# Performance work log

Measured on AMD Instinct MI355X. Metric: run time of the kernel, lower is better.

Reference implementation:

```python
import jax, jax.numpy as jnp
import numpy as np

N = 512   # speakers
M = 64    # samples per speaker
D = 768   # embedding dim
EPS = 1e-8  # torch F.cosine_similarity eps


def setup_inputs() -> dict:
    key = jax.random.key(0)
    k1, = jax.random.split(key, 1)
    speaker_vectors = jax.random.normal(k1, (N * M, D), dtype=jnp.float32)
    w = jnp.asarray(10.0, dtype=jnp.float32)
    b = jnp.asarray(-5.0, dtype=jnp.float32)
    return {"speaker_vectors": speaker_vectors, "w": w, "b": b}


def _cosine(a, b):
    # torch F.cosine_similarity: a.b / (max(|a|,eps) * max(|b|,eps)), over last dim
    na = jnp.maximum(jnp.linalg.norm(a, axis=-1), EPS)
    nb = jnp.maximum(jnp.linalg.norm(b, axis=-1), EPS)
    return jnp.sum(a * b, axis=-1) / (na * nb)


def reference(speaker_vectors, w, b):
    x = speaker_vectors.reshape(N, M, D)            # [N, M, D]
    sums = x.sum(axis=1)                            # [N, D]
    centroids = sums / M                            # [N, D]
    excl = (sums[:, None, :] - x) / (M - 1)         # exclusive centroids [N, M, D]

    # cosine sim of every centroid against every sample: [N_centroid, N_spk, M]
    xn = jnp.maximum(jnp.linalg.norm(x, axis=-1), EPS)          # [N, M]
    cn = jnp.maximum(jnp.linalg.norm(centroids, axis=-1), EPS)  # [N]
    dots = jnp.einsum('nd,imd->nim', centroids, x)              # [N, N, M]
    S = w * (dots / (cn[:, None, None] * xn[None])) + b         # [N, N, M]

    # same-speaker entries use the leave-one-out centroid
    S_same = w * _cosine(excl, x) + b               # [N, M]
    idx = jnp.arange(N)
    S = S.at[idx, idx].set(S_same)                  # overwrite diagonal block

    # L_j = -S_same_j + log sum_n exp(S[n, j])
    L = -S_same + jax.scipy.special.logsumexp(S, axis=0)  # [N, M]
    return L.sum()
```

## Files before the change

kernel.cpp:

```cpp
#include <hip/hip_runtime.h>
#include <hip/hip_bf16.h>
#include <math.h>

#define EPS 1e-8f

typedef __attribute__((ext_vector_type(2))) unsigned long ulongx2;
typedef __attribute__((ext_vector_type(4))) float floatx4;
typedef unsigned char uchar_t;

#define GPTR(p) ((const __attribute__((address_space(1))) void*)(p))
#define LPTR(p) ((__attribute__((address_space(3))) void*)(p))

__device__ __forceinline__ unsigned int pk4(float a, float b, float c, float d) {
  int v = __builtin_amdgcn_cvt_pk_fp8_f32(a, b, 0, false);
  v = __builtin_amdgcn_cvt_pk_fp8_f32(c, d, v, true);
  return (unsigned int)v;
}

__global__ __launch_bounds__(512, 4) void kA(const float* __restrict__ x,
    uchar_t* __restrict__ xbf8fm, float* __restrict__ sums_f32,
    float* __restrict__ ss, float* __restrict__ rcn,
    float* __restrict__ xx, float* __restrict__ rxn,
    const float* __restrict__ wp) {
  const int n = blockIdx.x;
  const int t = threadIdx.x;
  const int wv = t >> 6, l = t & 63;
  __shared__ uchar_t xs[64][776];
  __shared__ float rqp[64][65];
  __shared__ float red8[8];

  float4 cs[3] = {{0,0,0,0},{0,0,0,0},{0,0,0,0}};
  for (int c = 0; c < 2; ++c) {
    float4 v[4][3];
#pragma unroll
    for (int rr = 0; rr < 4; ++rr) {
      const int r = wv * 8 + c * 4 + rr;
      const float* rp = x + ((size_t)n * 64 + r) * 768 + l * 4;
#pragma unroll
      for (int q = 0; q < 3; ++q) v[rr][q] = *(const float4*)(rp + q * 256);
    }
#pragma unroll
    for (int rr = 0; rr < 4; ++rr) {
      const int r = wv * 8 + c * 4 + rr;
      float rq = 0.f;
#pragma unroll
      for (int q = 0; q < 3; ++q) {
        const float4 u = v[rr][q];
        *(unsigned int*)&xs[r][l * 4 + q * 256] = pk4(u.x, u.y, u.z, u.w);
        rq += u.x*u.x + u.y*u.y + u.z*u.z + u.w*u.w;
        cs[q].x += u.x; cs[q].y += u.y; cs[q].z += u.z; cs[q].w += u.w;
      }
      rqp[r][l] = rq;
    }
  }
  __syncthreads();

  {
    const int gg = wv >> 1;
    const int half = wv & 1;
    const int g = n * 4 + gg;
#pragma unroll
    for (int ksi = 0; ksi < 6; ++ksi) {
      const int ks = half * 6 + ksi;
      const uchar_t* sp = &xs[gg * 16 + (l & 15)][ks * 64 + (l >> 4) * 8];
      uint2 lo = *(const uint2*)sp;
      uint2 hi = *(const uint2*)(sp + 32);
      uint4 outv = {lo.x, lo.y, hi.x, hi.y};
      *(uint4*)(xbf8fm + (size_t)((g * 12 + ks) * 64 + l) * 16) = outv;
    }
  }

  {
    const int r = t >> 3;
    const int o = (t & 7) * 8;
    float s = 0.f;
#pragma unroll
    for (int i = 0; i < 8; ++i) s += rqp[r][o + i];
    s += __shfl_xor(s, 1, 64);
    s += __shfl_xor(s, 2, 64);
    s += __shfl_xor(s, 4, 64);
    if ((t & 7) == 0) {
      const int j = n * 64 + r;
      xx[j] = s;
      rxn[j] = 1.0f / fmaxf(sqrtf(s), EPS);
    }
  }
  __syncthreads();

  float (*csum)[768] = (float (*)[768])&xs[0][0];
#pragma unroll
  for (int q = 0; q < 3; ++q)
    *(floatx4*)&csum[wv][l * 4 + q * 256] = (floatx4){cs[q].x, cs[q].y, cs[q].z, cs[q].w};
  __syncthreads();

  float lss = 0.f;
  {
    const int c0 = t;
    float s0 = 0.f;
#pragma unroll
    for (int w = 0; w < 8; ++w) s0 += csum[w][c0];
    sums_f32[(size_t)n * 768 + c0] = s0;
    lss += s0 * s0;
    if (t < 256) {
      const int c1 = 512 + t;
      float s1 = 0.f;
#pragma unroll
      for (int w = 0; w < 8; ++w) s1 += csum[w][c1];
      sums_f32[(size_t)n * 768 + c1] = s1;
      lss += s1 * s1;
    }
  }
  for (int o = 32; o; o >>= 1) lss += __shfl_xor(lss, o, 64);
  if (l == 0) red8[wv] = lss;
  __syncthreads();
  if (t == 0) {
    float vv = 0.f;
#pragma unroll
    for (int w = 0; w < 8; ++w) vv += red8[w];
    ss[n] = vv;
    rcn[n] = (*wp) / fmaxf(sqrtf(vv), 64.f * EPS);
  }
}

__global__ __launch_bounds__(256) void kA2(const float* __restrict__ sums_f32,
    uchar_t* __restrict__ sums8fm) {
  const int g = blockIdx.x;
  const int wv = threadIdx.x >> 6, l = threadIdx.x & 63;
#pragma unroll
  for (int ksi = 0; ksi < 3; ++ksi) {
    const int ks = wv * 3 + ksi;
    const float* sp = sums_f32 + (size_t)(g * 16 + (l & 15)) * 768
                      + ks * 64 + (l >> 4) * 8;
    float4 a0 = *(const float4*)sp;
    float4 a1 = *(const float4*)(sp + 4);
    float4 b0 = *(const float4*)(sp + 32);
    float4 b1 = *(const float4*)(sp + 36);
    uint4 outv = { pk4(a0.x, a0.y, a0.z, a0.w), pk4(a1.x, a1.y, a1.z, a1.w),
                   pk4(b0.x, b0.y, b0.z, b0.w), pk4(b1.x, b1.y, b1.z, b1.w) };
    *(uint4*)(sums8fm + (size_t)((g * 12 + ks) * 64 + l) * 16) = outv;
  }
}

__global__ __launch_bounds__(512, 2) void kC(const uchar_t* __restrict__ xbf8fm,
    const uchar_t* __restrict__ sums8fm, const float* __restrict__ rcn,
    const float* __restrict__ rxn, float* __restrict__ colsum_part,
    float* __restrict__ sdiag_dot, const float* __restrict__ bp) {
  __shared__ uchar_t lds[4][32768];
  const int b = blockIdx.x;
  const int xcd = b & 7;
  const int inner = b >> 3;
  const int nt = inner & 1;
  const int jt = xcd + ((inner >> 1) << 3);
  const int n0 = nt * 256, j0 = jt * 256;
  const int t = threadIdx.x, wv = t >> 6, l = t & 63;
  const int wm = wv >> 2, wj = wv & 3;
  const int gA0 = n0 / 16, gB0 = j0 / 16;

#define STAGE(KS_, BUF_) {                                                     \
    const int fb0_ = wv * 2, fb1_ = wv * 2 + 1;                                \
    __builtin_amdgcn_global_load_lds(                                          \
        GPTR(sums8fm + (size_t)(((gA0 + fb0_) * 12 + (KS_)) * 64 + l) * 16),   \
        LPTR(&lds[BUF_][fb0_ * 1024]), 16, 0, 0);                              \
    __builtin_amdgcn_global_load_lds(                                          \
        GPTR(sums8fm + (size_t)(((gA0 + fb1_) * 12 + (KS_)) * 64 + l) * 16),   \
        LPTR(&lds[BUF_][fb1_ * 1024]), 16, 0, 0);                              \
    __builtin_amdgcn_global_load_lds(                                          \
        GPTR(xbf8fm + (size_t)(((gB0 + fb0_) * 12 + (KS_)) * 64 + l) * 16),    \
        LPTR(&lds[BUF_][16384 + fb0_ * 1024]), 16, 0, 0);                      \
    __builtin_amdgcn_global_load_lds(                                          \
        GPTR(xbf8fm + (size_t)(((gB0 + fb1_) * 12 + (KS_)) * 64 + l) * 16),    \
        LPTR(&lds[BUF_][16384 + fb1_ * 1024]), 16, 0, 0);                      \
  }

  floatx4 acc[8][4];
#pragma unroll
  for (int mi = 0; mi < 8; ++mi)
#pragma unroll
    for (int ni = 0; ni < 4; ++ni) acc[mi][ni] = (floatx4){0.f, 0.f, 0.f, 0.f};

  STAGE(0, 0)
  STAGE(1, 1)
  STAGE(2, 2)

  for (int kb = 0; kb < 12; ++kb) {
    if (kb < 10)       { asm volatile("s_waitcnt vmcnt(8)" ::: "memory"); }
    else if (kb == 10) { asm volatile("s_waitcnt vmcnt(4)" ::: "memory"); }
    else               { asm volatile("s_waitcnt vmcnt(0)" ::: "memory"); }
    __builtin_amdgcn_s_barrier();
    __builtin_amdgcn_sched_barrier(0);
    const int cb = kb & 3, sb = (kb + 3) & 3;

    ulongx2 af[8], bf[4];
#pragma unroll
    for (int ni = 0; ni < 4; ++ni)
      bf[ni] = *(const ulongx2*)&lds[cb][16384 + (wj * 4 + ni) * 1024 + l * 16];
#pragma unroll
    for (int mi = 0; mi < 8; ++mi)
      af[mi] = *(const ulongx2*)&lds[cb][(wm * 8 + mi) * 1024 + l * 16];
    if (kb + 3 < 12) STAGE(kb + 3, sb)
    __builtin_amdgcn_s_setprio(1);
#pragma unroll
    for (int mi = 0; mi < 8; ++mi)
#pragma unroll
      for (int ni = 0; ni < 4; ++ni) {
        acc[mi][ni] = __builtin_amdgcn_mfma_f32_16x16x32_fp8_fp8(
            (long)af[mi].x, (long)bf[ni].x, acc[mi][ni], 0, 0, 0);
        acc[mi][ni] = __builtin_amdgcn_mfma_f32_16x16x32_fp8_fp8(
            (long)af[mi].y, (long)bf[ni].y, acc[mi][ni], 0, 0, 0);
      }
    __builtin_amdgcn_s_setprio(0);
  }

  const float bb = *bp;
  float rxv[4], p[4] = {0.f, 0.f, 0.f, 0.f};
#pragma unroll
  for (int ni = 0; ni < 4; ++ni)
    rxv[ni] = rxn[j0 + wj * 64 + ni * 16 + (l & 15)];
  const bool diagblk = (nt == (jt >> 6));

#pragma unroll
  for (int mi = 0; mi < 8; ++mi) {
    float4 rr = *(const float4*)&rcn[n0 + wm * 128 + mi * 16 + ((l >> 4) << 2)];
    const float rc[4] = {rr.x, rr.y, rr.z, rr.w};
#pragma unroll
    for (int ni = 0; ni < 4; ++ni) {
      floatx4 a = acc[mi][ni];
#pragma unroll
      for (int q = 0; q < 4; ++q)
        p[ni] += __expf(a[q] * rc[q] * rxv[ni] + bb);
      if (diagblk) {
        const int jg = j0 + wj * 64 + ni * 16 + (l & 15);
#pragma unroll
        for (int q = 0; q < 4; ++q) {
          const int mg = n0 + wm * 128 + mi * 16 + ((l >> 4) << 2) + q;
          if (mg == (jg >> 6)) sdiag_dot[jg] = a[q];
        }
      }
    }
  }
#pragma unroll
  for (int ni = 0; ni < 4; ++ni) {
    p[ni] += __shfl_xor(p[ni], 16, 64);
    p[ni] += __shfl_xor(p[ni], 32, 64);
  }
  if (l < 16) {
    const int slot = nt * 2 + wm;
#pragma unroll
    for (int ni = 0; ni < 4; ++ni)
      colsum_part[(size_t)slot * 32768 + j0 + wj * 64 + ni * 16 + l] = p[ni];
  }
}

__global__ __launch_bounds__(256) void kD(const float* __restrict__ colsum_part,
    const float* __restrict__ sdiag_dot, const float* __restrict__ xx,
    const float* __restrict__ ss, const float* __restrict__ rcn,
    const float* __restrict__ wp, const float* __restrict__ bp,
    float* __restrict__ partial) {
  const int j = blockIdx.x * 256 + threadIdx.x;
  const int i = j >> 6;
  const float ww = *wp, bb = *bp;
  const float sx = sdiag_dot[j];
  const float xxv = xx[j];
  const float xn = fmaxf(sqrtf(xxv), EPS);
  const float rx = 1.0f / xn;
  const float sd = sx * rcn[i] * rx + bb;
  const float exn = sqrtf(fmaxf(ss[i] - 2.f * sx + xxv, 0.f)) * (1.f / 63.f);
  const float edot = (sx - xxv) * (1.f / 63.f);
  const float sm = ww * edot / (fmaxf(exn, EPS) * xn) + bb;
  const float cssum = colsum_part[j] + colsum_part[32768 + j]
                    + colsum_part[65536 + j] + colsum_part[98304 + j];
  const float tot = cssum - __expf(sd) + __expf(sm);
  float L = -sm + logf(fmaxf(tot, 1e-30f));
  for (int o = 32; o; o >>= 1) L += __shfl_xor(L, o, 64);
  __shared__ float red[4];
  if ((threadIdx.x & 63) == 0) red[threadIdx.x >> 6] = L;
  __syncthreads();
  if (threadIdx.x == 0)
    partial[blockIdx.x] = red[0] + red[1] + red[2] + red[3];
}

__global__ __launch_bounds__(128) void kE(const float* __restrict__ partial,
    float* __restrict__ out) {
  const int t = threadIdx.x;
  float v = partial[t];
  for (int o = 32; o; o >>= 1) v += __shfl_xor(v, o, 64);
  __shared__ float r2[2];
  if ((t & 63) == 0) r2[t >> 6] = v;
  __syncthreads();
  if (t == 0) out[0] = r2[0] + r2[1];
}

extern "C" void kernel_launch(void* const* d_in, const int* in_sizes, int n_in,
                              void* d_out, int out_size, void* d_ws, size_t ws_size,
                              hipStream_t stream) {
  const float* x  = (const float*)d_in[0];
  const float* wp = (const float*)d_in[1];
  const float* bp = (const float*)d_in[2];
  float* out = (float*)d_out;

  float* fws = (float*)d_ws;
  float* ss          = fws;
  float* rcn         = fws + 512;
  float* xx          = fws + 1024;
  float* rxn         = fws + 33792;
  float* colsum_part = fws + 66560;
  float* sdiag_dot   = fws + 197632;
  float* partial     = fws + 230400;
  float* sums_f32    = fws + 230528;
  uchar_t* sums8fm   = (uchar_t*)(fws + 623744);
  uchar_t* xbf8fm    = (uchar_t*)(fws + 722048);

  kA<<<512, 512, 0, stream>>>(x, xbf8fm, sums_f32, ss, rcn, xx, rxn, wp);
  kA2<<<32, 256, 0, stream>>>(sums_f32, sums8fm);
  kC<<<256, 512, 0, stream>>>(xbf8fm, sums8fm, rcn, rxn, colsum_part, sdiag_dot, bp);
  kD<<<128, 256, 0, stream>>>(colsum_part, sdiag_dot, xx, ss, rcn, wp, bp, partial);
  kE<<<1, 128, 0, stream>>>(partial, out);
}
```

Measured before the change: 52.12 us.

## Stream prep-kernel rows through double-buffered async global-to-LDS loads

The prep kernel now streams its 64 rows in eight chunks of 8 using global_load_lds DMA into a two-slot float LDS buffer. Each chunk is converted to fp8 and reduced (squared norms, column sums) while the next chunk loads, so memory latency overlaps with compute. The fp8 fragment-major stores move inside the loop, every 16 rows, using a smaller 16-row staging buffer. This adds LDS footprint, manual waitcnt and barrier handling, and extra barriers per pair of chunks, and it relies on per-wave buffer ownership being safe without full syncs.

```diff
diff --git a/kernel.cpp b/kernel.cpp
--- a/kernel.cpp
+++ b/kernel.cpp
@@ -25,48 +25,69 @@
   const int n = blockIdx.x;
   const int t = threadIdx.x;
   const int wv = t >> 6, l = t & 63;
-  __shared__ uchar_t xs[64][776];
+  __shared__ float fbuf[2][8][768];
+  __shared__ uchar_t xs[16][776];
   __shared__ float rqp[64][65];
   __shared__ float red8[8];
 
+  const float* xbase = x + (size_t)n * 64 * 768;
+
+#define DMA(C_) {                                                              \
+    const float* src_ = xbase + (size_t)((C_) * 8 + wv) * 768 + l * 4;         \
+    __builtin_amdgcn_global_load_lds(GPTR(src_),                               \
+        LPTR(&fbuf[(C_) & 1][wv][0]), 16, 0, 0);                               \
+    __builtin_amdgcn_global_load_lds(GPTR(src_ + 256),                         \
+        LPTR(&fbuf[(C_) & 1][wv][256]), 16, 0, 0);                             \
+    __builtin_amdgcn_global_load_lds(GPTR(src_ + 512),                         \
+        LPTR(&fbuf[(C_) & 1][wv][512]), 16, 0, 0);                             \
+  }
+
   float4 cs[3] = {{0,0,0,0},{0,0,0,0},{0,0,0,0}};
-  for (int c = 0; c < 2; ++c) {
-    float4 v[4][3];
-#pragma unroll
-    for (int rr = 0; rr < 4; ++rr) {
-      const int r = wv * 8 + c * 4 + rr;
-      const float* rp = x + ((size_t)n * 64 + r) * 768 + l * 4;
-#pragma unroll
-      for (int q = 0; q < 3; ++q) v[rr][q] = *(const float4*)(rp + q * 256);
-    }
-#pragma unroll
-    for (int rr = 0; rr < 4; ++rr) {
-      const int r = wv * 8 + c * 4 + rr;
-      float rq = 0.f;
-#pragma unroll
-      for (int q = 0; q < 3; ++q) {
-        const float4 u = v[rr][q];
-        *(unsigned int*)&xs[r][l * 4 + q * 256] = pk4(u.x, u.y, u.z, u.w);
-        rq += u.x*u.x + u.y*u.y + u.z*u.z + u.w*u.w;
-        cs[q].x += u.x; cs[q].y += u.y; cs[q].z += u.z; cs[q].w += u.w;
+  DMA(0)
+
+  for (int c = 0; c < 8; ++c) {
+    if (c < 7) { DMA(c + 1) asm volatile("s_waitcnt vmcnt(3)" ::: "memory"); }
+    else       { asm volatile("s_waitcnt vmcnt(0)" ::: "memory"); }
+    __builtin_amdgcn_sched_barrier(0);
+
+    {
+      const float* fr = &fbuf[c & 1][wv][0];
+      float4 v0 = *(const float4*)(fr + l * 4);
+      float4 v1 = *(const float4*)(fr + l * 4 + 256);
+      float4 v2 = *(const float4*)(fr + l * 4 + 512);
+      const int xr = (c & 1) * 8 + wv;
+      *(unsigned int*)&xs[xr][l * 4]       = pk4(v0.x, v0.y, v0.z, v0.w);
+      *(unsigned int*)&xs[xr][l * 4 + 256] = pk4(v1.x, v1.y, v1.z, v1.w);
+      *(unsigned int*)&xs[xr][l * 4 + 512] = pk4(v2.x, v2.y, v2.z, v2.w);
+      float rq = v0.x*v0.x + v0.y*v0.y + v0.z*v0.z + v0.w*v0.w
+               + v1.x*v1.x + v1.y*v1.y + v1.z*v1.z + v1.w*v1.w
+               + v2.x*v2.x + v2.y*v2.y + v2.z*v2.z + v2.w*v2.w;
+      rqp[c * 8 + wv][l] = rq;
+      cs[0].x += v0.x; cs[0].y += v0.y; cs[0].z += v0.z; cs[0].w += v0.w;
+      cs[1].x += v1.x; cs[1].y += v1.y; cs[1].z += v1.z; cs[1].w += v1.w;
+      cs[2].x += v2.x; cs[2].y += v2.y; cs[2].z += v2.z; cs[2].w += v2.w;
+    }
+
+    if (c & 1) {
+      asm volatile("s_waitcnt lgkmcnt(0)" ::: "memory");
+      __builtin_amdgcn_s_barrier();
+      const int g = n * 4 + (c >> 1);
+      {
+        const uchar_t* sp = &xs[l & 15][wv * 64 + (l >> 4) * 8];
+        uint2 lo = *(const uint2*)sp;
+        uint2 hi = *(const uint2*)(sp + 32);
+        uint4 outv = {lo.x, lo.y, hi.x, hi.y};
+        *(uint4*)(xbf8fm + (size_t)((g * 12 + wv) * 64 + l) * 16) = outv;
       }
-      rqp[r][l] = rq;
-    }
-  }
-  __syncthreads();
-
-  {
-    const int gg = wv >> 1;
-    const int half = wv & 1;
-    const int g = n * 4 + gg;
-#pragma unroll
-    for (int ksi = 0; ksi < 6; ++ksi) {
-      const int ks = half * 6 + ksi;
-      const uchar_t* sp = &xs[gg * 16 + (l & 15)][ks * 64 + (l >> 4) * 8];
-      uint2 lo = *(const uint2*)sp;
-      uint2 hi = *(const uint2*)(sp + 32);
-      uint4 outv = {lo.x, lo.y, hi.x, hi.y};
-      *(uint4*)(xbf8fm + (size_t)((g * 12 + ks) * 64 + l) * 16) = outv;
+      if (wv < 4) {
+        const int ks = 8 + wv;
+        const uchar_t* sp = &xs[l & 15][ks * 64 + (l >> 4) * 8];
+        uint2 lo = *(const uint2*)sp;
+        uint2 hi = *(const uint2*)(sp + 32);
+        uint4 outv = {lo.x, lo.y, hi.x, hi.y};
+        *(uint4*)(xbf8fm + (size_t)((g * 12 + ks) * 64 + l) * 16) = outv;
+      }
+      __builtin_amdgcn_s_barrier();
     }
   }
 
@@ -85,13 +106,13 @@
       rxn[j] = 1.0f / fmaxf(sqrtf(s), EPS);
     }
   }
-  __syncthreads();
-
-  float (*csum)[768] = (float (*)[768])&xs[0][0];
+
+  float (*csum)[768] = (float (*)[768])&fbuf[0][0][0];
 #pragma unroll
   for (int q = 0; q < 3; ++q)
     *(floatx4*)&csum[wv][l * 4 + q * 256] = (floatx4){cs[q].x, cs[q].y, cs[q].z, cs[q].w};
-  __syncthreads();
+  asm volatile("s_waitcnt lgkmcnt(0)" ::: "memory");
+  __builtin_amdgcn_s_barrier();
 
   float lss = 0.f;
   {
```

After: 53.15 us. No clear change (+2.0%).

## Halve kC centroid tile to 128 rows, double grid, switch to double-buffered LDS

Applied to the files above, without the earlier changes.

The GEMM kernel kC now computes 128x256 tiles instead of 256x256, which doubles the grid to 512 blocks so more CUs are busy and per-block register/LDS pressure drops. The LDS pipeline shrinks from a 4-deep to a 2-deep ring, with an extra barrier so each buffer is refilled right after fragments are read. colsum partials grow from 4 to 8 slices, and kD sums all 8. This trades more global loads of the sample operand and an extra barrier per k-step for higher occupancy and parallelism.

```diff
diff --git a/kernel.cpp b/kernel.cpp
--- a/kernel.cpp
+++ b/kernel.cpp
@@ -141,66 +141,67 @@
   }
 }
 
-__global__ __launch_bounds__(512, 2) void kC(const uchar_t* __restrict__ xbf8fm,
+__global__ __launch_bounds__(512) void kC(const uchar_t* __restrict__ xbf8fm,
     const uchar_t* __restrict__ sums8fm, const float* __restrict__ rcn,
     const float* __restrict__ rxn, float* __restrict__ colsum_part,
     float* __restrict__ sdiag_dot, const float* __restrict__ bp) {
-  __shared__ uchar_t lds[4][32768];
+  __shared__ uchar_t lds[2][24576];
   const int b = blockIdx.x;
   const int xcd = b & 7;
   const int inner = b >> 3;
-  const int nt = inner & 1;
-  const int jt = xcd + ((inner >> 1) << 3);
-  const int n0 = nt * 256, j0 = jt * 256;
+  const int nt = inner & 3;
+  const int jt = xcd + ((inner >> 2) << 3);
+  const int n0 = nt * 128, j0 = jt * 256;
   const int t = threadIdx.x, wv = t >> 6, l = t & 63;
   const int wm = wv >> 2, wj = wv & 3;
-  const int gA0 = n0 / 16, gB0 = j0 / 16;
+  const int gA0 = n0 >> 4, gB0 = j0 >> 4;
 
 #define STAGE(KS_, BUF_) {                                                     \
-    const int fb0_ = wv * 2, fb1_ = wv * 2 + 1;                                \
-    __builtin_amdgcn_global_load_lds(                                          \
-        GPTR(sums8fm + (size_t)(((gA0 + fb0_) * 12 + (KS_)) * 64 + l) * 16),   \
-        LPTR(&lds[BUF_][fb0_ * 1024]), 16, 0, 0);                              \
-    __builtin_amdgcn_global_load_lds(                                          \
-        GPTR(sums8fm + (size_t)(((gA0 + fb1_) * 12 + (KS_)) * 64 + l) * 16),   \
-        LPTR(&lds[BUF_][fb1_ * 1024]), 16, 0, 0);                              \
-    __builtin_amdgcn_global_load_lds(                                          \
-        GPTR(xbf8fm + (size_t)(((gB0 + fb0_) * 12 + (KS_)) * 64 + l) * 16),    \
-        LPTR(&lds[BUF_][16384 + fb0_ * 1024]), 16, 0, 0);                      \
-    __builtin_amdgcn_global_load_lds(                                          \
-        GPTR(xbf8fm + (size_t)(((gB0 + fb1_) * 12 + (KS_)) * 64 + l) * 16),    \
-        LPTR(&lds[BUF_][16384 + fb1_ * 1024]), 16, 0, 0);                      \
-  }
-
-  floatx4 acc[8][4];
-#pragma unroll
-  for (int mi = 0; mi < 8; ++mi)
+    _Pragma("unroll")                                                          \
+    for (int i_ = 0; i_ < 3; ++i_) {                                           \
+      const int bl_ = wv * 3 + i_;                                             \
+      if (bl_ < 8) {                                                           \
+        __builtin_amdgcn_global_load_lds(                                      \
+            GPTR(sums8fm + (size_t)(((gA0 + bl_) * 12 + (KS_)) * 64 + l) * 16),\
+            LPTR(&lds[BUF_][bl_ * 1024 + l * 16]), 16, 0, 0);                  \
+      } else {                                                                 \
+        __builtin_amdgcn_global_load_lds(                                      \
+            GPTR(xbf8fm + (size_t)(((gB0 + bl_ - 8) * 12 + (KS_)) * 64 + l) * 16), \
+            LPTR(&lds[BUF_][bl_ * 1024 + l * 16]), 16, 0, 0);                  \
+      }                                                                        \
+    }                                                                          \
+  }
+
+  floatx4 acc[4][4];
+#pragma unroll
+  for (int mi = 0; mi < 4; ++mi)
 #pragma unroll
     for (int ni = 0; ni < 4; ++ni) acc[mi][ni] = (floatx4){0.f, 0.f, 0.f, 0.f};
 
   STAGE(0, 0)
   STAGE(1, 1)
-  STAGE(2, 2)
 
   for (int kb = 0; kb < 12; ++kb) {
-    if (kb < 10)       { asm volatile("s_waitcnt vmcnt(8)" ::: "memory"); }
-    else if (kb == 10) { asm volatile("s_waitcnt vmcnt(4)" ::: "memory"); }
-    else               { asm volatile("s_waitcnt vmcnt(0)" ::: "memory"); }
+    if (kb < 11) { asm volatile("s_waitcnt vmcnt(3)" ::: "memory"); }
+    else         { asm volatile("s_waitcnt vmcnt(0)" ::: "memory"); }
     __builtin_amdgcn_s_barrier();
     __builtin_amdgcn_sched_barrier(0);
-    const int cb = kb & 3, sb = (kb + 3) & 3;
-
-    ulongx2 af[8], bf[4];
+    const int cb = kb & 1;
+
+    ulongx2 af[4], bf[4];
+#pragma unroll
+    for (int mi = 0; mi < 4; ++mi)
+      af[mi] = *(const ulongx2*)&lds[cb][(wm * 4 + mi) * 1024 + l * 16];
 #pragma unroll
     for (int ni = 0; ni < 4; ++ni)
-      bf[ni] = *(const ulongx2*)&lds[cb][16384 + (wj * 4 + ni) * 1024 + l * 16];
-#pragma unroll
-    for (int mi = 0; mi < 8; ++mi)
-      af[mi] = *(const ulongx2*)&lds[cb][(wm * 8 + mi) * 1024 + l * 16];
-    if (kb + 3 < 12) STAGE(kb + 3, sb)
+      bf[ni] = *(const ulongx2*)&lds[cb][8192 + (wj * 4 + ni) * 1024 + l * 16];
+    asm volatile("s_waitcnt lgkmcnt(0)" ::: "memory");
+    __builtin_amdgcn_s_barrier();
+    __builtin_amdgcn_sched_barrier(0);
+    if (kb + 2 < 12) STAGE(kb + 2, cb)
     __builtin_amdgcn_s_setprio(1);
 #pragma unroll
-    for (int mi = 0; mi < 8; ++mi)
+    for (int mi = 0; mi < 4; ++mi)
 #pragma unroll
       for (int ni = 0; ni < 4; ++ni) {
         acc[mi][ni] = __builtin_amdgcn_mfma_f32_16x16x32_fp8_fp8(
@@ -216,11 +217,11 @@
 #pragma unroll
   for (int ni = 0; ni < 4; ++ni)
     rxv[ni] = rxn[j0 + wj * 64 + ni * 16 + (l & 15)];
-  const bool diagblk = (nt == (jt >> 6));
-
-#pragma unroll
-  for (int mi = 0; mi < 8; ++mi) {
-    float4 rr = *(const float4*)&rcn[n0 + wm * 128 + mi * 16 + ((l >> 4) << 2)];
+  const bool diagblk = (nt == (jt >> 5));
+
+#pragma unroll
+  for (int mi = 0; mi < 4; ++mi) {
+    float4 rr = *(const float4*)&rcn[n0 + wm * 64 + mi * 16 + ((l >> 4) << 2)];
     const float rc[4] = {rr.x, rr.y, rr.z, rr.w};
 #pragma unroll
     for (int ni = 0; ni < 4; ++ni) {
@@ -232,7 +233,7 @@
         const int jg = j0 + wj * 64 + ni * 16 + (l & 15);
 #pragma unroll
         for (int q = 0; q < 4; ++q) {
-          const int mg = n0 + wm * 128 + mi * 16 + ((l >> 4) << 2) + q;
+          const int mg = n0 + wm * 64 + mi * 16 + ((l >> 4) << 2) + q;
           if (mg == (jg >> 6)) sdiag_dot[jg] = a[q];
         }
       }
@@ -267,8 +268,9 @@
   const float exn = sqrtf(fmaxf(ss[i] - 2.f * sx + xxv, 0.f)) * (1.f / 63.f);
   const float edot = (sx - xxv) * (1.f / 63.f);
   const float sm = ww * edot / (fmaxf(exn, EPS) * xn) + bb;
-  const float cssum = colsum_part[j] + colsum_part[32768 + j]
-                    + colsum_part[65536 + j] + colsum_part[98304 + j];
+  float cssum = 0.f;
+#pragma unroll
+  for (int s = 0; s < 8; ++s) cssum += colsum_part[(size_t)s * 32768 + j];
   const float tot = cssum - __expf(sd) + __expf(sm);
   float L = -sm + logf(fmaxf(tot, 1e-30f));
   for (int o = 32; o; o >>= 1) L += __shfl_xor(L, o, 64);
@@ -304,15 +306,15 @@
   float* xx          = fws + 1024;
   float* rxn         = fws + 33792;
   float* colsum_part = fws + 66560;
-  float* sdiag_dot   = fws + 197632;
-  float* partial     = fws + 230400;
-  float* sums_f32    = fws + 230528;
-  uchar_t* sums8fm   = (uchar_t*)(fws + 623744);
-  uchar_t* xbf8fm    = (uchar_t*)(fws + 722048);
+  float* sdiag_dot   = fws + 328704;
+  float* partial     = fws + 361472;
+  float* sums_f32    = fws + 361600;
+  uchar_t* sums8fm   = (uchar_t*)(fws + 754816);
+  uchar_t* xbf8fm    = (uchar_t*)(fws + 853120);
 
   kA<<<512, 512, 0, stream>>>(x, xbf8fm, sums_f32, ss, rcn, xx, rxn, wp);
   kA2<<<32, 256, 0, stream>>>(sums_f32, sums8fm);
-  kC<<<256, 512, 0, stream>>>(xbf8fm, sums8fm, rcn, rxn, colsum_part, sdiag_dot, bp);
+  kC<<<512, 512, 0, stream>>>(xbf8fm, sums8fm, rcn, rxn, colsum_part, sdiag_dot, bp);
   kD<<<128, 256, 0, stream>>>(colsum_part, sdiag_dot, xx, ss, rcn, wp, bp, partial);
   kE<<<1, 128, 0, stream>>>(partial, out);
 }
```

Measured after the change: 51.76 us, median of 2. About the same (-0.7%).
